# Performance work log

Hardware: AMD Instinct MI355X
Metric: run time of the kernel (lower is better)

## Reference

```python
import jax, jax.numpy as jnp
import numpy as np

N, E = 50000, 800000
IN_C, HID, HEADS, LAT = 128, 64, 2, 32
NEG_SLOPE = 0.2  # PyG GATConv default LeakyReLU slope


def gat_layer(x, src, dst, W, att_src, att_dst, bias, heads, out_ch, concat, n):
    # Linear projection, per-head: [n, heads, out_ch]
    h = (x @ W).reshape(n, heads, out_ch)
    a_src = jnp.einsum('nhc,hc->nh', h, att_src)  # [n, heads]
    a_dst = jnp.einsum('nhc,hc->nh', h, att_dst)
    # Per-edge attention logits (edge j->i uses src j, dst i)
    alpha = jax.nn.leaky_relu(a_src[src] + a_dst[dst], negative_slope=NEG_SLOPE)  # [e, heads]
    # Segment softmax over incoming edges of each destination node
    amax = jax.ops.segment_max(alpha, dst, num_segments=n)
    ealpha = jnp.exp(alpha - amax[dst])
    denom = jax.ops.segment_sum(ealpha, dst, num_segments=n)
    alpha = ealpha / (denom[dst] + 1e-16)
    # Weighted scatter-aggregate of source features
    msg = h[src] * alpha[:, :, None]  # [e, heads, out_ch]
    out = jax.ops.segment_sum(msg, dst, num_segments=n)  # [n, heads, out_ch]
    out = out.reshape(n, heads * out_ch) if concat else out.mean(axis=1)
    return out + bias


def setup_inputs() -> dict:
    key = jax.random.key(0)
    ks = jax.random.split(key, 16)
    x = jax.random.normal(ks[0], (N, IN_C), dtype=jnp.float32)
    edge_index = jax.random.randint(ks[1], (2, E), 0, N, dtype=jnp.int32).astype(jnp.int64)
    s = 0.1
    W1 = jax.random.normal(ks[2], (IN_C, HEADS * HID), dtype=jnp.float32) * s
    att_src1 = jax.random.normal(ks[3], (HEADS, HID), dtype=jnp.float32) * s
    att_dst1 = jax.random.normal(ks[4], (HEADS, HID), dtype=jnp.float32) * s
    b1 = jnp.zeros((HEADS * HID,), dtype=jnp.float32)
    Wmu = jax.random.normal(ks[5], (HEADS * HID, LAT), dtype=jnp.float32) * s
    att_src_mu = jax.random.normal(ks[6], (1, LAT), dtype=jnp.float32) * s
    att_dst_mu = jax.random.normal(ks[7], (1, LAT), dtype=jnp.float32) * s
    bmu = jnp.zeros((LAT,), dtype=jnp.float32)
    Wlv = jax.random.normal(ks[8], (HEADS * HID, LAT), dtype=jnp.float32) * s
    att_src_lv = jax.random.normal(ks[9], (1, LAT), dtype=jnp.float32) * s
    att_dst_lv = jax.random.normal(ks[10], (1, LAT), dtype=jnp.float32) * s
    blv = jnp.zeros((LAT,), dtype=jnp.float32)
    return {"x": x, "edge_index": edge_index, "W1": W1, "att_src1": att_src1,
            "att_dst1": att_dst1, "b1": b1, "Wmu": Wmu, "att_src_mu": att_src_mu,
            "att_dst_mu": att_dst_mu, "bmu": bmu, "Wlv": Wlv,
            "att_src_lv": att_src_lv, "att_dst_lv": att_dst_lv, "blv": blv}


def reference(x, edge_index, W1, att_src1, att_dst1, b1,
              Wmu, att_src_mu, att_dst_mu, bmu,
              Wlv, att_src_lv, att_dst_lv, blv):
    n = x.shape[0]
    # PyG GATConv adds self-loops by default
    loops = jnp.arange(n, dtype=edge_index.dtype)
    src = jnp.concatenate([edge_index[0], loops])
    dst = jnp.concatenate([edge_index[1], loops])
    h = gat_layer(x, src, dst, W1, att_src1, att_dst1, b1, HEADS, HID, True, n)
    h = jax.nn.elu(h)
    mu = gat_layer(h, src, dst, Wmu, att_src_mu, att_dst_mu, bmu, 1, LAT, False, n)
    logvar = gat_layer(h, src, dst, Wlv, att_src_lv, att_dst_lv, blv, 1, LAT, False, n)
    return (mu, logvar)
```

## Files before the change

kernel.cpp:

```cpp
#include <hip/hip_runtime.h>
#include <hip/hip_bf16.h>

#define N_NODES 50000
#define N_EDGES 800000
#define EP (N_EDGES + N_NODES)
#define IN_C 128
#define HID 64
#define HEADS 2
#define LAT 32
#define NEG_SLOPE 0.2f
#define MAXDEG 256
#define NBUCKET 391
#define BCAP 3072
#define CHUNK 2048
#define NSCAT ((EP + CHUNK - 1) / CHUNK)
#define NPROJ1 ((N_NODES + 31) / 32)

typedef __attribute__((ext_vector_type(8))) short bf16x8;
typedef __attribute__((ext_vector_type(4))) float f32x4;

__device__ __forceinline__ unsigned short f2bf(float f) {
  unsigned u = __float_as_uint(f);
  u += 0x7FFF + ((u >> 16) & 1);
  return (unsigned short)(u >> 16);
}
__device__ __forceinline__ float bf_lo(unsigned u) { return __uint_as_float(u << 16); }
__device__ __forceinline__ float bf_hi(unsigned u) { return __uint_as_float(u & 0xFFFF0000u); }

__device__ __forceinline__ bf16x8 pack_bf8(const float* __restrict__ p) {
  float4 a = *(const float4*)p;
  float4 b = *(const float4*)(p + 4);
  bf16x8 r;
  r[0] = (short)f2bf(a.x); r[1] = (short)f2bf(a.y);
  r[2] = (short)f2bf(a.z); r[3] = (short)f2bf(a.w);
  r[4] = (short)f2bf(b.x); r[5] = (short)f2bf(b.y);
  r[6] = (short)f2bf(b.z); r[7] = (short)f2bf(b.w);
  return r;
}

__global__ __launch_bounds__(256) void prep_kernel(
    const float* __restrict__ W1, const float* __restrict__ Wmu,
    const float* __restrict__ Wlv, int* __restrict__ cursor,
    unsigned short* __restrict__ Wb1g, unsigned short* __restrict__ Wb2g) {
  const int b = blockIdx.x, t = threadIdx.x;
  if (b == 0) {
    for (int i = t; i < NBUCKET; i += 256) cursor[i] = 0;
  } else if (b <= 64) {
    int i = (b - 1) * 256 + t;
    int k = i >> 7, n = i & 127;
    int kk = k >> 5, q = (k >> 3) & 3, j = k & 7;
    Wb1g[((((kk << 2) + q) << 7) + n) * 8 + j] = f2bf(W1[i]);
  } else {
    int i = (b - 65) * 256 + t;
    int k = i >> 6, n = i & 63;
    float v = (n < 32) ? Wmu[k * 32 + n] : Wlv[k * 32 + (n - 32)];
    int kk = k >> 5, q = (k >> 3) & 3, j = k & 7;
    Wb2g[((((kk << 2) + q) << 6) + n) * 8 + j] = f2bf(v);
  }
}

struct ScatSmem {
  int histL[512];
  int baseL[512];
  int gbaseL[512];
  int wsumS[4];
  int nvalS;
  unsigned staging[CHUNK];
  unsigned short bktidL[CHUNK];
};
union K1Smem { ScatSmem sc; float part[32][4]; };

__global__ __launch_bounds__(256) void k1_kernel(
    const int* __restrict__ ei, int* __restrict__ cursor,
    unsigned* __restrict__ csr,
    const float* __restrict__ x, const unsigned short* __restrict__ Wb1g,
    const float* __restrict__ att_src, const float* __restrict__ att_dst,
    unsigned short* __restrict__ h1b, float* __restrict__ a1) {
  __shared__ K1Smem sm;
  const int t = threadIdx.x, lane = t & 63, wid = t >> 6;

  if (blockIdx.x < NSCAT) {
    for (int i = t; i < 512; i += 256) sm.sc.histL[i] = 0;
    __syncthreads();
    int myb[CHUNK / 256];
    int myloc[CHUNK / 256];
    unsigned mypay[CHUNK / 256];
    #pragma unroll
    for (int i = 0; i < CHUNK / 256; ++i) {
      int e = blockIdx.x * CHUNK + i * 256 + t;
      if (e < EP) {
        int s, d;
        if (e < N_EDGES) { s = ei[e]; d = ei[N_EDGES + e]; }
        else { s = d = e - N_EDGES; }
        int b = d >> 7;
        myb[i] = b;
        mypay[i] = ((unsigned)(d & 127) << 17) | (unsigned)s;
        myloc[i] = atomicAdd(&sm.sc.histL[b], 1);
      } else myb[i] = -1;
    }
    __syncthreads();
    {
      int v0 = sm.sc.histL[2 * t], v1 = sm.sc.histL[2 * t + 1];
      int pair = v0 + v1, inc = pair;
      #pragma unroll
      for (int off = 1; off < 64; off <<= 1) {
        int nv = __shfl_up(inc, off);
        if (lane >= off) inc += nv;
      }
      if (lane == 63) sm.sc.wsumS[wid] = inc;
      __syncthreads();
      if (t == 0) {
        int run = 0;
        #pragma unroll
        for (int w = 0; w < 4; ++w) { int c = sm.sc.wsumS[w]; sm.sc.wsumS[w] = run; run += c; }
        sm.sc.nvalS = run;
      }
      __syncthreads();
      int excl = sm.sc.wsumS[wid] + inc - pair;
      sm.sc.baseL[2 * t] = excl;
      sm.sc.baseL[2 * t + 1] = excl + v0;
    }
    __syncthreads();
    #pragma unroll
    for (int i = 0; i < CHUNK / 256; ++i)
      if (myb[i] >= 0) {
        int p = sm.sc.baseL[myb[i]] + myloc[i];
        sm.sc.staging[p] = mypay[i];
        sm.sc.bktidL[p] = (unsigned short)myb[i];
      }
    for (int b = t; b < NBUCKET; b += 256) {
      int c = sm.sc.histL[b];
      sm.sc.gbaseL[b] = c ? atomicAdd(&cursor[b], c) : 0;
    }
    __syncthreads();
    const int nval = sm.sc.nvalS;
    for (int j = t; j < nval; j += 256) {
      int b = sm.sc.bktidL[j];
      int off = sm.sc.gbaseL[b] + (j - sm.sc.baseL[b]);
      if (off < BCAP) csr[b * BCAP + off] = sm.sc.staging[j];
    }
  } else {
    const int pb = blockIdx.x - NSCAT;
    if (t < 128) ((float*)sm.part)[t] = 0.f;
    __syncthreads();
    const int w = wid;
    const int m = lane & 15, quad = lane >> 4;
    const int row0 = pb * 32;
    const int n0 = w * 32;
    const int head = w >> 1;
    f32x4 acc[2][2] = {};
    #pragma unroll
    for (int kk = 0; kk < 4; ++kk) {
      bf16x8 afr[2], bfr[2];
      #pragma unroll
      for (int mt = 0; mt < 2; ++mt) {
        int row = row0 + mt * 16 + m;
        if (row >= N_NODES) row = N_NODES - 1;
        afr[mt] = pack_bf8(x + (size_t)row * 128 + kk * 32 + quad * 8);
      }
      #pragma unroll
      for (int nt = 0; nt < 2; ++nt)
        bfr[nt] = *(const bf16x8*)&Wb1g[((((kk << 2) + quad) << 7) + n0 + nt * 16 + m) * 8];
      #pragma unroll
      for (int mt = 0; mt < 2; ++mt)
        #pragma unroll
        for (int nt = 0; nt < 2; ++nt)
          acc[mt][nt] = __builtin_amdgcn_mfma_f32_16x16x32_bf16(
              afr[mt], bfr[nt], acc[mt][nt], 0, 0, 0);
    }
    float asv[2], adv[2];
    #pragma unroll
    for (int nt = 0; nt < 2; ++nt) {
      int cc = ((n0 & 63) + nt * 16 + m);
      asv[nt] = att_src[head * HID + cc];
      adv[nt] = att_dst[head * HID + cc];
    }
    #pragma unroll
    for (int mt = 0; mt < 2; ++mt)
      #pragma unroll
      for (int r = 0; r < 4; ++r) {
        int row = row0 + mt * 16 + quad * 4 + r;
        if (row < N_NODES) {
          #pragma unroll
          for (int nt = 0; nt < 2; ++nt)
            h1b[(size_t)row * 128 + n0 + nt * 16 + m] = f2bf(acc[mt][nt][r]);
        }
        float s = acc[mt][0][r] * asv[0] + acc[mt][1][r] * asv[1];
        float d = acc[mt][0][r] * adv[0] + acc[mt][1][r] * adv[1];
        #pragma unroll
        for (int off = 8; off; off >>= 1) {
          s += __shfl_xor(s, off);
          d += __shfl_xor(d, off);
        }
        if (m == 0) {
          atomicAdd(&sm.part[mt * 16 + quad * 4 + r][head], s);
          atomicAdd(&sm.part[mt * 16 + quad * 4 + r][2 + head], d);
        }
      }
    __syncthreads();
    if (t < 32) {
      int row = row0 + t;
      if (row < N_NODES)
        *(float4*)&a1[(size_t)row * 4] = make_float4(
            sm.part[t][0], sm.part[t][1], sm.part[t][2], sm.part[t][3]);
    }
  }
}

__global__ __launch_bounds__(256) void bucket_fill_kernel(
    const int* __restrict__ cursor, unsigned* __restrict__ csr,
    int* __restrict__ counts, int* __restrict__ cend) {
  __shared__ unsigned eseg[BCAP];
  __shared__ int hist[128];
  __shared__ int basef[128];
  __shared__ int cur[128];
  const int b = blockIdx.x, t = threadIdx.x;
  const int segbase = b * BCAP;
  int cnt = cursor[b];
  if (cnt > BCAP) cnt = BCAP;
  if (t < 128) hist[t] = 0;
  __syncthreads();
  for (int j = t; j < cnt; j += 256) {
    unsigned u = csr[segbase + j];
    eseg[j] = u;
    atomicAdd(&hist[u >> 17], 1);
  }
  __syncthreads();
  if (t < 64) {
    int v0 = hist[2 * t], v1 = hist[2 * t + 1];
    int pair = v0 + v1, inc = pair;
    #pragma unroll
    for (int off = 1; off < 64; off <<= 1) {
      int nv = __shfl_up(inc, off);
      if (t >= off) inc += nv;
    }
    int excl = inc - pair;
    basef[2 * t] = excl;
    basef[2 * t + 1] = excl + v0;
  }
  __syncthreads();
  if (t < 128) {
    cur[t] = basef[t];
    int n = b * 128 + t;
    if (n < N_NODES) {
      counts[n] = hist[t];
      cend[n] = segbase + basef[t] + hist[t];
    }
  }
  __syncthreads();
  for (int j = t; j < cnt; j += 256) {
    unsigned u = eseg[j];
    int dl = u >> 17;
    int p = atomicAdd(&cur[dl], 1);
    csr[segbase + p] = u & 0x1FFFF;
  }
}

__global__ __launch_bounds__(64) void agg1_csr_kernel(
    const int* __restrict__ counts, const int* __restrict__ cend,
    const unsigned* __restrict__ csr_src, const float4* __restrict__ a1,
    const unsigned* __restrict__ h1b2, const float* __restrict__ b,
    float* __restrict__ hact) {
  __shared__ float w_lds[2][MAXDEG];
  __shared__ int   s_lds[MAXDEG];
  const int n = blockIdx.x;
  const int t = threadIdx.x;
  const int end = cend[n];
  int cnt = counts[n];
  if (cnt > MAXDEG) cnt = MAXDEG;
  const int beg = end - cnt;
  const float4 bv = a1[n];
  float p0 = 0.f, p1 = 0.f;
  for (int i = t; i < cnt; i += 64) {
    int s = (int)csr_src[beg + i];
    float4 av = a1[s];
    float l0 = av.x + bv.z; l0 = l0 > 0.f ? l0 : NEG_SLOPE * l0;
    float l1 = av.y + bv.w; l1 = l1 > 0.f ? l1 : NEG_SLOPE * l1;
    float e0 = expf(l0), e1 = expf(l1);
    w_lds[0][i] = e0; w_lds[1][i] = e1; s_lds[i] = s;
    p0 += e0; p1 += e1;
  }
  #pragma unroll
  for (int off = 32; off; off >>= 1) {
    p0 += __shfl_xor(p0, off);
    p1 += __shfl_xor(p1, off);
  }
  __syncthreads();
  const int head = t >> 5;
  const unsigned* hp = h1b2 + t;
  float ax = 0.f, ay = 0.f;
  #pragma unroll 4
  for (int i = 0; i < cnt; ++i) {
    int s = s_lds[i];
    float w = w_lds[head][i];
    unsigned u = hp[(size_t)s * 64];
    ax += bf_lo(u) * w; ay += bf_hi(u) * w;
  }
  float inv = 1.f / ((head ? p1 : p0) + 1e-16f);
  float vx = ax * inv + b[t * 2];
  float vy = ay * inv + b[t * 2 + 1];
  vx = vx > 0.f ? vx : (expf(vx) - 1.f);
  vy = vy > 0.f ? vy : (expf(vy) - 1.f);
  *(float2*)(hact + (size_t)n * 128 + t * 2) = make_float2(vx, vy);
}

__global__ __launch_bounds__(256) void proj2_kernel(
    const float* __restrict__ h, const unsigned short* __restrict__ Wb2g,
    const float* __restrict__ asmu, const float* __restrict__ admu,
    const float* __restrict__ aslv, const float* __restrict__ adlv,
    unsigned short* __restrict__ h2b, float* __restrict__ a2) {
  const int t = threadIdx.x;
  const int w = t >> 6, lane = t & 63;
  const int m = lane & 15, quad = lane >> 4;
  const int row0 = blockIdx.x * 64 + (w >> 1) * 32;
  const int j = w & 1;
  const int n0 = j * 32;
  f32x4 acc[2][2] = {};
  #pragma unroll
  for (int kk = 0; kk < 4; ++kk) {
    bf16x8 afr[2], bfr[2];
    #pragma unroll
    for (int mt = 0; mt < 2; ++mt) {
      int row = row0 + mt * 16 + m;
      if (row >= N_NODES) row = N_NODES - 1;
      afr[mt] = pack_bf8(h + (size_t)row * 128 + kk * 32 + quad * 8);
    }
    #pragma unroll
    for (int nt = 0; nt < 2; ++nt)
      bfr[nt] = *(const bf16x8*)&Wb2g[((((kk << 2) + quad) << 6) + n0 + nt * 16 + m) * 8];
    #pragma unroll
    for (int mt = 0; mt < 2; ++mt)
      #pragma unroll
      for (int nt = 0; nt < 2; ++nt)
        acc[mt][nt] = __builtin_amdgcn_mfma_f32_16x16x32_bf16(
            afr[mt], bfr[nt], acc[mt][nt], 0, 0, 0);
  }
  float asv[2], adv[2];
  #pragma unroll
  for (int nt = 0; nt < 2; ++nt) {
    int o = nt * 16 + m;
    asv[nt] = (j ? aslv : asmu)[o];
    adv[nt] = (j ? adlv : admu)[o];
  }
  #pragma unroll
  for (int mt = 0; mt < 2; ++mt)
    #pragma unroll
    for (int r = 0; r < 4; ++r) {
      int row = row0 + mt * 16 + quad * 4 + r;
      if (row < N_NODES) {
        #pragma unroll
        for (int nt = 0; nt < 2; ++nt)
          h2b[(size_t)row * 64 + n0 + nt * 16 + m] = f2bf(acc[mt][nt][r]);
      }
      float s = acc[mt][0][r] * asv[0] + acc[mt][1][r] * asv[1];
      float d = acc[mt][0][r] * adv[0] + acc[mt][1][r] * adv[1];
      #pragma unroll
      for (int off = 8; off; off >>= 1) {
        s += __shfl_xor(s, off);
        d += __shfl_xor(d, off);
      }
      if (m == 0 && row < N_NODES) {
        a2[(size_t)row * 4 + j * 2 + 0] = s;
        a2[(size_t)row * 4 + j * 2 + 1] = d;
      }
    }
}

__global__ __launch_bounds__(64) void agg2_csr_kernel(
    const int* __restrict__ counts, const int* __restrict__ cend,
    const unsigned* __restrict__ csr_src, const float4* __restrict__ a2,
    const unsigned* __restrict__ h2b2,
    const float* __restrict__ bmu, const float* __restrict__ blv,
    float* __restrict__ out) {
  __shared__ float w_lds[2][2][MAXDEG];
  __shared__ int   s_lds[2][MAXDEG];
  const int t = threadIdx.x, half = t >> 5, hl = t & 31;
  const int n = blockIdx.x * 2 + half;
  const int end = cend[n];
  int cnt = counts[n];
  if (cnt > MAXDEG) cnt = MAXDEG;
  const int beg = end - cnt;
  const float4 bv = a2[n];
  float p0 = 0.f, p1 = 0.f;
  for (int i = hl; i < cnt; i += 32) {
    int s = (int)csr_src[beg + i];
    float4 av = a2[s];
    float l0 = av.x + bv.y; l0 = l0 > 0.f ? l0 : NEG_SLOPE * l0;
    float l1 = av.z + bv.w; l1 = l1 > 0.f ? l1 : NEG_SLOPE * l1;
    float e0 = expf(l0), e1 = expf(l1);
    w_lds[half][0][i] = e0; w_lds[half][1][i] = e1; s_lds[half][i] = s;
    p0 += e0; p1 += e1;
  }
  #pragma unroll
  for (int off = 16; off; off >>= 1) {
    p0 += __shfl_xor(p0, off);
    p1 += __shfl_xor(p1, off);
  }
  __syncthreads();
  const int c0 = 2 * hl;
  const int j = c0 >> 5;
  const int o = c0 & 31;
  const unsigned* hp = h2b2 + hl;
  float ax = 0.f, ay = 0.f;
  #pragma unroll 4
  for (int i = 0; i < cnt; ++i) {
    int s = s_lds[half][i];
    float w = w_lds[half][j][i];
    unsigned u = hp[(size_t)s * 32];
    ax += bf_lo(u) * w; ay += bf_hi(u) * w;
  }
  float inv = 1.f / ((j ? p1 : p0) + 1e-16f);
  const float* bb = j ? blv : bmu;
  *(float2*)&out[(size_t)j * N_NODES * LAT + (size_t)n * LAT + o] =
      make_float2(ax * inv + bb[o], ay * inv + bb[o + 1]);
}

extern "C" void kernel_launch(void* const* d_in, const int* in_sizes, int n_in,
                              void* d_out, int out_size, void* d_ws, size_t ws_size,
                              hipStream_t stream) {
  const float* x        = (const float*)d_in[0];
  const int* ei         = (const int*)d_in[1];
  const float* W1       = (const float*)d_in[2];
  const float* att_src1 = (const float*)d_in[3];
  const float* att_dst1 = (const float*)d_in[4];
  const float* b1       = (const float*)d_in[5];
  const float* Wmu      = (const float*)d_in[6];
  const float* asmu     = (const float*)d_in[7];
  const float* admu     = (const float*)d_in[8];
  const float* bmu      = (const float*)d_in[9];
  const float* Wlv      = (const float*)d_in[10];
  const float* aslv     = (const float*)d_in[11];
  const float* adlv     = (const float*)d_in[12];
  const float* blv      = (const float*)d_in[13];
  float* out = (float*)d_out;

  float* ws   = (float*)d_ws;
  float* hact = ws;
  float* a1   = hact + (size_t)N_NODES * 128;
  float* a2   = a1 + (size_t)N_NODES * 4;
  unsigned short* h1b = (unsigned short*)(a2 + (size_t)N_NODES * 4);
  unsigned short* h2b = h1b + (size_t)N_NODES * 128;
  unsigned short* Wb1g = h2b + (size_t)N_NODES * 64;
  unsigned short* Wb2g = Wb1g + 16384;
  int* counts = (int*)(Wb2g + 8192);
  int* cend   = counts + N_NODES;
  int* cursor = cend + N_NODES;
  unsigned* csr = (unsigned*)(cursor + NBUCKET);

  prep_kernel<<<97, 256, 0, stream>>>(W1, Wmu, Wlv, cursor, Wb1g, Wb2g);

  k1_kernel<<<NSCAT + NPROJ1, 256, 0, stream>>>(
      ei, cursor, csr, x, Wb1g, att_src1, att_dst1, h1b, a1);
  bucket_fill_kernel<<<NBUCKET, 256, 0, stream>>>(cursor, csr, counts, cend);
  agg1_csr_kernel<<<N_NODES, 64, 0, stream>>>(
      counts, cend, csr, (const float4*)a1, (const unsigned*)h1b, b1, hact);
  proj2_kernel<<<(N_NODES + 63) / 64, 256, 0, stream>>>(
      hact, Wb2g, asmu, admu, aslv, adlv, h2b, a2);
  agg2_csr_kernel<<<N_NODES / 2, 64, 0, stream>>>(
      counts, cend, csr, (const float4*)a2, (const unsigned*)h2b, bmu, blv, out);
}
```

Measured before the change: 210.9 us.

## Restructure GAT aggregation kernels to vectorized 16B gathers with edge-parallel lane groups

```diff
diff --git a/kernel.cpp b/kernel.cpp
--- a/kernel.cpp
+++ b/kernel.cpp
@@ -256,28 +256,29 @@
   }
 }
 
-__global__ __launch_bounds__(64) void agg1_csr_kernel(
+__global__ __launch_bounds__(256) void agg1_csr_kernel(
     const int* __restrict__ counts, const int* __restrict__ cend,
     const unsigned* __restrict__ csr_src, const float4* __restrict__ a1,
     const unsigned* __restrict__ h1b2, const float* __restrict__ b,
     float* __restrict__ hact) {
-  __shared__ float w_lds[2][MAXDEG];
-  __shared__ int   s_lds[MAXDEG];
-  const int n = blockIdx.x;
-  const int t = threadIdx.x;
+  __shared__ float2 w_lds[4][MAXDEG];
+  __shared__ int   s_lds[4][MAXDEG];
+  const int t = threadIdx.x, wid = t >> 6, lane = t & 63;
+  const int n = blockIdx.x * 4 + wid;
   const int end = cend[n];
   int cnt = counts[n];
   if (cnt > MAXDEG) cnt = MAXDEG;
   const int beg = end - cnt;
   const float4 bv = a1[n];
   float p0 = 0.f, p1 = 0.f;
-  for (int i = t; i < cnt; i += 64) {
+  for (int i = lane; i < cnt; i += 64) {
     int s = (int)csr_src[beg + i];
     float4 av = a1[s];
     float l0 = av.x + bv.z; l0 = l0 > 0.f ? l0 : NEG_SLOPE * l0;
     float l1 = av.y + bv.w; l1 = l1 > 0.f ? l1 : NEG_SLOPE * l1;
     float e0 = expf(l0), e1 = expf(l1);
-    w_lds[0][i] = e0; w_lds[1][i] = e1; s_lds[i] = s;
+    w_lds[wid][i] = make_float2(e0, e1);
+    s_lds[wid][i] = s;
     p0 += e0; p1 += e1;
   }
   #pragma unroll
@@ -286,22 +287,37 @@
     p1 += __shfl_xor(p1, off);
   }
   __syncthreads();
-  const int head = t >> 5;
-  const unsigned* hp = h1b2 + t;
-  float ax = 0.f, ay = 0.f;
-  #pragma unroll 4
-  for (int i = 0; i < cnt; ++i) {
-    int s = s_lds[i];
-    float w = w_lds[head][i];
-    unsigned u = hp[(size_t)s * 64];
-    ax += bf_lo(u) * w; ay += bf_hi(u) * w;
-  }
-  float inv = 1.f / ((head ? p1 : p0) + 1e-16f);
-  float vx = ax * inv + b[t * 2];
-  float vy = ay * inv + b[t * 2 + 1];
-  vx = vx > 0.f ? vx : (expf(vx) - 1.f);
-  vy = vy > 0.f ? vy : (expf(vy) - 1.f);
-  *(float2*)(hact + (size_t)n * 128 + t * 2) = make_float2(vx, vy);
+  const int g = lane >> 4;
+  const int lq = lane & 15;
+  const int head = lq >> 3;
+  float acc[8] = {0.f, 0.f, 0.f, 0.f, 0.f, 0.f, 0.f, 0.f};
+  #pragma unroll 2
+  for (int i = g; i < cnt; i += 4) {
+    int s = s_lds[wid][i];
+    float w = ((const float*)&w_lds[wid][i])[head];
+    uint4 u = *(const uint4*)(h1b2 + (size_t)s * 64 + lq * 4);
+    acc[0] += bf_lo(u.x) * w; acc[1] += bf_hi(u.x) * w;
+    acc[2] += bf_lo(u.y) * w; acc[3] += bf_hi(u.y) * w;
+    acc[4] += bf_lo(u.z) * w; acc[5] += bf_hi(u.z) * w;
+    acc[6] += bf_lo(u.w) * w; acc[7] += bf_hi(u.w) * w;
+  }
+  #pragma unroll
+  for (int j = 0; j < 8; ++j) {
+    acc[j] += __shfl_xor(acc[j], 16);
+    acc[j] += __shfl_xor(acc[j], 32);
+  }
+  if (g == 0) {
+    float inv = 1.f / ((head ? p1 : p0) + 1e-16f);
+    float o[8];
+    #pragma unroll
+    for (int j = 0; j < 8; ++j) {
+      float v = acc[j] * inv + b[lq * 8 + j];
+      o[j] = v > 0.f ? v : (expf(v) - 1.f);
+    }
+    float4* dst = (float4*)(hact + (size_t)n * 128 + lq * 8);
+    dst[0] = make_float4(o[0], o[1], o[2], o[3]);
+    dst[1] = make_float4(o[4], o[5], o[6], o[7]);
+  }
 }
 
 __global__ __launch_bounds__(256) void proj2_kernel(
@@ -366,53 +382,69 @@
     }
 }
 
-__global__ __launch_bounds__(64) void agg2_csr_kernel(
+__global__ __launch_bounds__(256) void agg2_csr_kernel(
     const int* __restrict__ counts, const int* __restrict__ cend,
     const unsigned* __restrict__ csr_src, const float4* __restrict__ a2,
     const unsigned* __restrict__ h2b2,
     const float* __restrict__ bmu, const float* __restrict__ blv,
     float* __restrict__ out) {
-  __shared__ float w_lds[2][2][MAXDEG];
-  __shared__ int   s_lds[2][MAXDEG];
-  const int t = threadIdx.x, half = t >> 5, hl = t & 31;
-  const int n = blockIdx.x * 2 + half;
+  __shared__ float2 w_lds[4][MAXDEG];
+  __shared__ int   s_lds[4][MAXDEG];
+  const int t = threadIdx.x, wid = t >> 6, lane = t & 63;
+  const int n = blockIdx.x * 4 + wid;
   const int end = cend[n];
   int cnt = counts[n];
   if (cnt > MAXDEG) cnt = MAXDEG;
   const int beg = end - cnt;
   const float4 bv = a2[n];
   float p0 = 0.f, p1 = 0.f;
-  for (int i = hl; i < cnt; i += 32) {
+  for (int i = lane; i < cnt; i += 64) {
     int s = (int)csr_src[beg + i];
     float4 av = a2[s];
     float l0 = av.x + bv.y; l0 = l0 > 0.f ? l0 : NEG_SLOPE * l0;
     float l1 = av.z + bv.w; l1 = l1 > 0.f ? l1 : NEG_SLOPE * l1;
     float e0 = expf(l0), e1 = expf(l1);
-    w_lds[half][0][i] = e0; w_lds[half][1][i] = e1; s_lds[half][i] = s;
+    w_lds[wid][i] = make_float2(e0, e1);
+    s_lds[wid][i] = s;
     p0 += e0; p1 += e1;
   }
   #pragma unroll
-  for (int off = 16; off; off >>= 1) {
+  for (int off = 32; off; off >>= 1) {
     p0 += __shfl_xor(p0, off);
     p1 += __shfl_xor(p1, off);
   }
   __syncthreads();
-  const int c0 = 2 * hl;
-  const int j = c0 >> 5;
-  const int o = c0 & 31;
-  const unsigned* hp = h2b2 + hl;
-  float ax = 0.f, ay = 0.f;
-  #pragma unroll 4
-  for (int i = 0; i < cnt; ++i) {
-    int s = s_lds[half][i];
-    float w = w_lds[half][j][i];
-    unsigned u = hp[(size_t)s * 32];
-    ax += bf_lo(u) * w; ay += bf_hi(u) * w;
-  }
-  float inv = 1.f / ((j ? p1 : p0) + 1e-16f);
-  const float* bb = j ? blv : bmu;
-  *(float2*)&out[(size_t)j * N_NODES * LAT + (size_t)n * LAT + o] =
-      make_float2(ax * inv + bb[o], ay * inv + bb[o + 1]);
+  const int g = lane >> 3;
+  const int lq = lane & 7;
+  const int j = lq >> 2;
+  float acc[8] = {0.f, 0.f, 0.f, 0.f, 0.f, 0.f, 0.f, 0.f};
+  #pragma unroll 2
+  for (int i = g; i < cnt; i += 8) {
+    int s = s_lds[wid][i];
+    float w = ((const float*)&w_lds[wid][i])[j];
+    uint4 u = *(const uint4*)(h2b2 + (size_t)s * 32 + lq * 4);
+    acc[0] += bf_lo(u.x) * w; acc[1] += bf_hi(u.x) * w;
+    acc[2] += bf_lo(u.y) * w; acc[3] += bf_hi(u.y) * w;
+    acc[4] += bf_lo(u.z) * w; acc[5] += bf_hi(u.z) * w;
+    acc[6] += bf_lo(u.w) * w; acc[7] += bf_hi(u.w) * w;
+  }
+  #pragma unroll
+  for (int jj = 0; jj < 8; ++jj) {
+    acc[jj] += __shfl_xor(acc[jj], 8);
+    acc[jj] += __shfl_xor(acc[jj], 16);
+    acc[jj] += __shfl_xor(acc[jj], 32);
+  }
+  if (g == 0) {
+    float inv = 1.f / ((j ? p1 : p0) + 1e-16f);
+    const float* bb = j ? blv : bmu;
+    const int o = (lq & 3) * 8;
+    float r[8];
+    #pragma unroll
+    for (int jj = 0; jj < 8; ++jj) r[jj] = acc[jj] * inv + bb[o + jj];
+    float4* dst = (float4*)(out + (size_t)j * N_NODES * LAT + (size_t)n * LAT + o);
+    dst[0] = make_float4(r[0], r[1], r[2], r[3]);
+    dst[1] = make_float4(r[4], r[5], r[6], r[7]);
+  }
 }
 
 extern "C" void kernel_launch(void* const* d_in, const int* in_sizes, int n_in,
@@ -452,10 +484,10 @@
   k1_kernel<<<NSCAT + NPROJ1, 256, 0, stream>>>(
       ei, cursor, csr, x, Wb1g, att_src1, att_dst1, h1b, a1);
   bucket_fill_kernel<<<NBUCKET, 256, 0, stream>>>(cursor, csr, counts, cend);
-  agg1_csr_kernel<<<N_NODES, 64, 0, stream>>>(
+  agg1_csr_kernel<<<N_NODES / 4, 256, 0, stream>>>(
       counts, cend, csr, (const float4*)a1, (const unsigned*)h1b, b1, hact);
   proj2_kernel<<<(N_NODES + 63) / 64, 256, 0, stream>>>(
       hact, Wb2g, asmu, admu, aslv, adlv, h2b, a2);
-  agg2_csr_kernel<<<N_NODES / 2, 64, 0, stream>>>(
+  agg2_csr_kernel<<<N_NODES / 4, 256, 0, stream>>>(
       counts, cend, csr, (const float4*)a2, (const unsigned*)h2b, bmu, blv, out);
 }
```

Result: slower. 217.3 us (+3.0%).
